# Optimization experiments

Measured on AMD Instinct MI355X. Metric: run time of the kernel, lower is better.

## Reference

```python
import jax, jax.numpy as jnp
import numpy as np

H, I, B = 256, 128, 512

def setup_inputs() -> dict:
    key = jax.random.key(0)
    ks = jax.random.split(key, 24)
    n = lambda k, shp, s=1.0: jax.random.normal(k, shp, dtype=jnp.float32) * s
    inp = {
        "x": n(ks[0], (B, I)),
        "hx": n(ks[1], (B, H), 0.1),
        "cx": n(ks[2], (B, H, H), 0.1),
        # input->gate weights (hidden, input), xavier-like scale
        "Wii": n(ks[3], (H, I), (2.0 / (H + I)) ** 0.5),
        "Wif": n(ks[4], (H, I), (2.0 / (H + I)) ** 0.5),
        "Wig": n(ks[5], (H, I), (2.0 / (H + I)) ** 0.5),
        "Wio": n(ks[6], (H, I), (2.0 / (H + I)) ** 0.5),
        # hidden->gate weights (hidden, hidden), ~orthogonal scale
        "Whi": n(ks[7], (H, H), H ** -0.5),
        "Whit": n(ks[8], (H, H), H ** -0.5),
        "Whf": n(ks[9], (H, H), H ** -0.5),
        "Whft": n(ks[10], (H, H), H ** -0.5),
        "Whc": n(ks[11], (H, H), H ** -0.5),
        "Whct": n(ks[12], (H, H), H ** -0.5),
        "Who": n(ks[13], (H, H), H ** -0.5),
        "Uinv": n(ks[14], (H, H), H ** -0.5),
        "Vtinv": n(ks[15], (H, H), H ** -0.5),
        # biases: bi/bf/bg are full (H,H) matrices, bo is (H,1)
        "bi": jnp.zeros((H, H), jnp.float32),
        "bf": jnp.zeros((H, H), jnp.float32),
        "bg": jnp.zeros((H, H), jnp.float32),
        "bo": jnp.zeros((H, 1), jnp.float32),
    }
    return inp


def reference(x, hx, cx, Wii, Wif, Wig, Wio, Whi, Whit, Whf, Whft, Whc, Whct, Who, Uinv, Vtinv, bi, bf, bg, bo):
    # W @ diag(v) @ M^T  ==  einsum('hi,bi,gi->bhg', W, v, M)
    def sandwich(Wx, Wh, Wht, b):
        # (Wx*x) @ Wx^T + (Wh*hx) @ Wht^T + b  -> (B,H,H)
        xt = jnp.einsum('hi,bi,gi->bhg', Wx, x, Wx)
        ht = jnp.einsum('hj,bj,gj->bhg', Wh, hx, Wht)
        return xt + ht + b

    i = jax.nn.sigmoid(sandwich(Wii, Whi, Whit, bi))
    f = jax.nn.sigmoid(sandwich(Wif, Whf, Whft, bf))
    g = jnp.tanh(sandwich(Wig, Whc, Whct, bg))
    # o: ordinary vector gate (B,H)
    o = jax.nn.sigmoid(jnp.einsum('hi,bi->bh', Wio, x)
                       + jnp.einsum('hj,bj->bh', Who, hx) + bo[:, 0])
    cx_new = f * cx + i * g                     # (B,H,H)
    # diag(Uinv @ cx_new @ Vtinv) per batch element -> (B,H)
    proj_down = jnp.einsum('ij,bjk,ki->bi', Uinv, cx_new, Vtinv)
    hx_new = o * jax.nn.sigmoid(proj_down)
    return hx_new
```

## Files before the change

### kernel.cpp

```cpp
#include <hip/hip_runtime.h>

#define Hh 256
#define Ii 128
#define Bb 512
#define KF 384
#define KB 64
#define LDB 40

typedef __attribute__((ext_vector_type(8))) short bf16x8;
typedef __attribute__((ext_vector_type(4))) float f32x4;
typedef unsigned short u16;
typedef unsigned int u32;

__device__ inline float bf2f(u16 u) { return __uint_as_float(((u32)u) << 16); }
__device__ inline u16 f2bf(float f) {
  u32 u = __float_as_uint(f);
  u += 0x7FFFu + ((u >> 16) & 1u);
  return (u16)(u >> 16);
}
__device__ inline float sigm(float x) { return 1.0f / (1.0f + __expf(-x)); }
__device__ inline float tanh_f(float x) { return 1.0f - 2.0f / (1.0f + __expf(2.0f * x)); }

__device__ inline int sp_idx(int j, int kk) {
  return j * 64 + ((((kk >> 3) ^ (j & 7)) << 3) | (kk & 7));
}

__global__ __launch_bounds__(256) void k_prep(
    const float* __restrict__ Wii, const float* __restrict__ Wif, const float* __restrict__ Wig,
    const float* __restrict__ Whi, const float* __restrict__ Whit,
    const float* __restrict__ Whf, const float* __restrict__ Whft,
    const float* __restrict__ Whc, const float* __restrict__ Whct,
    const float* __restrict__ Vtinv,
    u16* __restrict__ RW, u16* __restrict__ CW, u16* __restrict__ Vtt,
    float* __restrict__ proj) {
  const int tid = threadIdx.x, bx = blockIdx.x, y = blockIdx.y;
  if (y < 3) {
    const float* WX  = (y == 0) ? Wii : (y == 1 ? Wif : Wig);
    const float* WHr = (y == 0) ? Whi : (y == 1 ? Whf : Whc);
    const float* WHt = (y == 0) ? Whit : (y == 1 ? Whft : Whct);
    u16* rw = RW + y * Hh * KF;
    u16* cw = CW + y * Hh * KF;
#pragma unroll
    for (int it = 0; it < 4; ++it) {
      int idx = it * 24576 + bx * 256 + tid;
      int h = idx / KF, t = idx - h * KF;
      float a, c;
      if (t < Ii) { a = WX[h * Ii + t]; c = a; }
      else        { a = WHr[h * Hh + t - Ii]; c = WHt[h * Hh + t - Ii]; }
      rw[idx] = f2bf(a);
      cw[idx] = f2bf(c);
    }
  } else if (bx < 64) {
    __shared__ u16 tbuf[32][33];
    const int c = tid & 31, r8 = tid >> 5;
    const int tr = bx >> 3, tc = bx & 7;
#pragma unroll
    for (int rr = r8; rr < 32; rr += 8)
      tbuf[rr][c] = f2bf(Vtinv[(tc * 32 + rr) * Hh + tr * 32 + c]);
    __syncthreads();
#pragma unroll
    for (int rr = r8; rr < 32; rr += 8)
      Vtt[(tr * 32 + rr) * Hh + tc * 32 + c] = tbuf[c][rr];
  } else {
    const int base = (bx - 64) * 256 + tid;
    const float4 z = {0.f, 0.f, 0.f, 0.f};
#pragma unroll
    for (int it = 0; it < 4; ++it)
      *(float4*)(proj + (size_t)(it * 8192 + base) * 4) = z;
  }
}

template <int PHASE>
__device__ __forceinline__ void gate_pass(
    const u16* __restrict__ rw, const u16* __restrict__ cw,
    const float* __restrict__ bias, const float* __restrict__ cx_b,
    u16* sP, u16* sB, const float* sV, int tid, int k0) {
  const int lane = tid & 63, w = tid >> 6;
  const int r15 = lane & 15, quad = lane >> 4;
  const int brow = tid >> 2, bcg = tid & 3;

  f32x4 acc[4][4];
#pragma unroll
  for (int ti = 0; ti < 4; ++ti)
#pragma unroll
    for (int tk = 0; tk < 4; ++tk)
#pragma unroll
      for (int r = 0; r < 4; ++r) acc[ti][tk][r] = 0.0f;

  uint4 bnx = *(const uint4*)(cw + (k0 + brow) * KF + bcg * 8);
  bf16x8 fa[4];
#pragma unroll
  for (int ti = 0; ti < 4; ++ti)
    fa[ti] = *(const bf16x8*)(rw + (w * 64 + ti * 16 + r15) * KF + quad * 8);
  if (PHASE == 0) __syncthreads();
  {
    union { uint4 v; u16 u[8]; } in, ov;
    in.v = bnx;
    const float4 v0 = *(const float4*)(&sV[bcg * 8]);
    const float4 v1 = *(const float4*)(&sV[bcg * 8 + 4]);
    const float vs[8] = {v0.x, v0.y, v0.z, v0.w, v1.x, v1.y, v1.z, v1.w};
#pragma unroll
    for (int e = 0; e < 8; ++e) ov.u[e] = f2bf(bf2f(in.u[e]) * vs[e]);
    *(uint4*)(sB + brow * LDB + bcg * 8) = ov.v;
  }
  __syncthreads();

#pragma unroll
  for (int kc = 0; kc < 12; ++kc) {
    const int cur = kc & 1, nxt = cur ^ 1;
    uint4 bnx2;
    bf16x8 fan[4];
    if (kc < 11) {
      bnx2 = *(const uint4*)(cw + (k0 + brow) * KF + (kc + 1) * 32 + bcg * 8);
#pragma unroll
      for (int ti = 0; ti < 4; ++ti)
        fan[ti] = *(const bf16x8*)(rw + (w * 64 + ti * 16 + r15) * KF + (kc + 1) * 32 + quad * 8);
    }
    bf16x8 fb[4];
#pragma unroll
    for (int tk = 0; tk < 4; ++tk)
      fb[tk] = *(const bf16x8*)(&sB[cur * (KB * LDB) + (tk * 16 + r15) * LDB + quad * 8]);
#pragma unroll
    for (int ti = 0; ti < 4; ++ti)
#pragma unroll
      for (int tk = 0; tk < 4; ++tk)
        acc[ti][tk] = __builtin_amdgcn_mfma_f32_16x16x32_bf16(fa[ti], fb[tk], acc[ti][tk], 0, 0, 0);
    if (kc < 11) {
      union { uint4 v; u16 u[8]; } in, ov;
      in.v = bnx2;
      const float4 v0 = *(const float4*)(&sV[(kc + 1) * 32 + bcg * 8]);
      const float4 v1 = *(const float4*)(&sV[(kc + 1) * 32 + bcg * 8 + 4]);
      const float vs[8] = {v0.x, v0.y, v0.z, v0.w, v1.x, v1.y, v1.z, v1.w};
#pragma unroll
      for (int e = 0; e < 8; ++e) ov.u[e] = f2bf(bf2f(in.u[e]) * vs[e]);
      *(uint4*)(sB + nxt * (KB * LDB) + brow * LDB + bcg * 8) = ov.v;
#pragma unroll
      for (int ti = 0; ti < 4; ++ti) fa[ti] = fan[ti];
    }
    __syncthreads();
  }

#pragma unroll
  for (int ti = 0; ti < 4; ++ti) {
#pragma unroll
    for (int tk = 0; tk < 4; ++tk) {
#pragma unroll
      for (int r = 0; r < 4; ++r) {
        const int j = w * 64 + ti * 16 + quad * 4 + r;
        const int kk = tk * 16 + r15;
        const int si = sp_idx(j, kk);
        float z = acc[ti][tk][r] + bias[j * Hh + k0 + kk];
        if (PHASE == 0) {
          sP[si] = f2bf(tanh_f(z));
        } else if (PHASE == 1) {
          sP[si] = f2bf(sigm(z) * bf2f(sP[si]));
        } else {
          sP[si] = f2bf(sigm(z) * cx_b[j * Hh + k0 + kk] + bf2f(sP[si]));
        }
      }
    }
  }
}

__global__ __launch_bounds__(256, 3) void k_main(
    const float* __restrict__ x, const float* __restrict__ hx, const float* __restrict__ cx,
    const float* __restrict__ bi, const float* __restrict__ bfm, const float* __restrict__ bg,
    const float* __restrict__ Uinv, const u16* __restrict__ RW, const u16* __restrict__ CW,
    const u16* __restrict__ Vtt, float* __restrict__ proj) {
  __shared__ u16 sP[Hh * 64];
  __shared__ u16 sB[2 * KB * LDB];
  __shared__ float sV[KF];

  const int tid  = threadIdx.x;
  const int b    = blockIdx.x >> 2;
  const int k0   = (blockIdx.x & 3) * KB;
  const int lane = tid & 63;
  const int w    = tid >> 6;
  const int r15  = lane & 15;
  const int quad = lane >> 4;

  if (tid < Ii) sV[tid] = x[b * Ii + tid];
  sV[Ii + tid] = hx[b * Hh + tid];

  const float* cx_b = cx + (size_t)b * Hh * Hh;
  gate_pass<0>(RW + 2 * Hh * KF, CW + 2 * Hh * KF, bg,  cx_b, sP, sB, sV, tid, k0);
  gate_pass<1>(RW + 0 * Hh * KF, CW + 0 * Hh * KF, bi,  cx_b, sP, sB, sV, tid, k0);
  gate_pass<2>(RW + 1 * Hh * KF, CW + 1 * Hh * KF, bfm, cx_b, sP, sB, sV, tid, k0);

  __syncthreads();

  bf16x8 va[4][2];
#pragma unroll
  for (int ti = 0; ti < 4; ++ti)
#pragma unroll
    for (int ks = 0; ks < 2; ++ks)
      va[ti][ks] = *(const bf16x8*)(Vtt + (w * 64 + ti * 16 + r15) * Hh + k0 + ks * 32 + quad * 8);

  float racc[4][4];
#pragma unroll
  for (int ti = 0; ti < 4; ++ti)
#pragma unroll
    for (int r = 0; r < 4; ++r) racc[ti][r] = 0.0f;

  for (int jt = 0; jt < 4; ++jt) {
    f32x4 pacc[4][4];
#pragma unroll
    for (int ti = 0; ti < 4; ++ti)
#pragma unroll
      for (int tj = 0; tj < 4; ++tj)
#pragma unroll
        for (int r = 0; r < 4; ++r) pacc[ti][tj][r] = 0.0f;
#pragma unroll
    for (int ks = 0; ks < 2; ++ks) {
      bf16x8 fbp[4];
#pragma unroll
      for (int tj = 0; tj < 4; ++tj) {
        const int j = jt * 64 + tj * 16 + r15;
        const int ch = (ks * 4 + quad) ^ (j & 7);
        fbp[tj] = *(const bf16x8*)(&sP[j * 64 + ch * 8]);
      }
#pragma unroll
      for (int ti = 0; ti < 4; ++ti)
#pragma unroll
        for (int tj = 0; tj < 4; ++tj)
          pacc[ti][tj] = __builtin_amdgcn_mfma_f32_16x16x32_bf16(va[ti][ks], fbp[tj], pacc[ti][tj], 0, 0, 0);
    }
#pragma unroll
    for (int ti = 0; ti < 4; ++ti)
#pragma unroll
      for (int tj = 0; tj < 4; ++tj)
#pragma unroll
        for (int r = 0; r < 4; ++r) {
          const int i  = w * 64 + ti * 16 + quad * 4 + r;
          const int jj = jt * 64 + tj * 16 + r15;
          racc[ti][r] += pacc[ti][tj][r] * Uinv[i * Hh + jj];
        }
  }

#pragma unroll
  for (int ti = 0; ti < 4; ++ti)
#pragma unroll
    for (int r = 0; r < 4; ++r) {
      float v = racc[ti][r];
      v += __shfl_xor(v, 1);
      v += __shfl_xor(v, 2);
      v += __shfl_xor(v, 4);
      v += __shfl_xor(v, 8);
      if (r15 == 0) atomicAdd(&proj[b * Hh + w * 64 + ti * 16 + quad * 4 + r], v);
    }
}

__global__ __launch_bounds__(256) void k_out(
    const float* __restrict__ x, const float* __restrict__ hx,
    const float* __restrict__ Wio, const float* __restrict__ Who,
    const float* __restrict__ bo, const float* __restrict__ proj,
    float* __restrict__ out) {
  __shared__ float sv[KF];
  const int b = blockIdx.x, tid = threadIdx.x;
  const int lane = tid & 63, w = tid >> 6;
  if (tid < Ii) sv[tid] = x[b * Ii + tid];
  sv[Ii + tid] = hx[b * Hh + tid];
  __syncthreads();
  for (int rr = 0; rr < 64; ++rr) {
    const int h = w * 64 + rr;
    float p = Wio[h * Ii + lane]        * sv[lane]
            + Wio[h * Ii + 64 + lane]   * sv[64 + lane]
            + Who[h * Hh + lane]        * sv[128 + lane]
            + Who[h * Hh + 64 + lane]   * sv[192 + lane]
            + Who[h * Hh + 128 + lane]  * sv[256 + lane]
            + Who[h * Hh + 192 + lane]  * sv[320 + lane];
    p += __shfl_xor(p, 32);
    p += __shfl_xor(p, 16);
    p += __shfl_xor(p, 8);
    p += __shfl_xor(p, 4);
    p += __shfl_xor(p, 2);
    p += __shfl_xor(p, 1);
    if (lane == 0)
      out[b * Hh + h] = sigm(p + bo[h]) * sigm(proj[b * Hh + h]);
  }
}

extern "C" void kernel_launch(void* const* d_in, const int* in_sizes, int n_in,
                              void* d_out, int out_size, void* d_ws, size_t ws_size,
                              hipStream_t stream) {
  (void)in_sizes; (void)n_in; (void)out_size; (void)ws_size;
  const float* x    = (const float*)d_in[0];
  const float* hx   = (const float*)d_in[1];
  const float* cx   = (const float*)d_in[2];
  const float* Wii  = (const float*)d_in[3];
  const float* Wif  = (const float*)d_in[4];
  const float* Wig  = (const float*)d_in[5];
  const float* Wio  = (const float*)d_in[6];
  const float* Whi  = (const float*)d_in[7];
  const float* Whit = (const float*)d_in[8];
  const float* Whf  = (const float*)d_in[9];
  const float* Whft = (const float*)d_in[10];
  const float* Whc  = (const float*)d_in[11];
  const float* Whct = (const float*)d_in[12];
  const float* Who  = (const float*)d_in[13];
  const float* Uinv = (const float*)d_in[14];
  const float* Vtinv= (const float*)d_in[15];
  const float* bi   = (const float*)d_in[16];
  const float* bf   = (const float*)d_in[17];
  const float* bg   = (const float*)d_in[18];
  const float* bo   = (const float*)d_in[19];
  float* out = (float*)d_out;

  u16* RW  = (u16*)d_ws;
  u16* CW  = RW + 3 * Hh * KF;
  u16* Vtt = CW + 3 * Hh * KF;
  float* proj = (float*)(Vtt + Hh * Hh);

  k_prep<<<dim3(96, 4), 256, 0, stream>>>(Wii, Wif, Wig, Whi, Whit, Whf, Whft, Whc, Whct,
                                          Vtinv, RW, CW, Vtt, proj);
  k_main<<<2048, 256, 0, stream>>>(x, hx, cx, bi, bf, bg, Uinv, RW, CW, Vtt, proj);
  k_out<<<512, 256, 0, stream>>>(x, hx, Wio, Who, bo, proj, out);
}
```

Before: 582.7 us.

## Split gate rows across blocks, keep gate state in registers, prepack bias

Each k_main block now covers 128 gate rows instead of 256, so the grid doubles and shared memory per block halves, allowing four blocks per CU. Intermediate gate values (tanh g, i*g) now stay in registers across phases rather than being written to and reread from shared memory. Biases are converted once to bf16 in the prep kernel and stored in a per-thread fragment order, so each thread reads them as vector loads. Costs are twice the atomics on proj, duplicated B-operand staging in each block, and bf16 rounding of the bias.

New measurement: 868.6 us. +49.1%, slower.

```diff
diff --git a/kernel.cpp b/kernel.cpp
--- a/kernel.cpp
+++ b/kernel.cpp
@@ -1,4 +1,5 @@
 #include <hip/hip_runtime.h>
+#include <hip/hip_bf16.h>
 
 #define Hh 256
 #define Ii 128
@@ -18,6 +19,10 @@
   u += 0x7FFFu + ((u >> 16) & 1u);
   return (u16)(u >> 16);
 }
+__device__ inline u32 pack_bf16x2(float a, float b) {
+  __hip_bfloat162 h = __float22bfloat162_rn(make_float2(a, b));
+  u32 r; __builtin_memcpy(&r, &h, 4); return r;
+}
 __device__ inline float sigm(float x) { return 1.0f / (1.0f + __expf(-x)); }
 __device__ inline float tanh_f(float x) { return 1.0f - 2.0f / (1.0f + __expf(2.0f * x)); }
 
@@ -31,8 +36,9 @@
     const float* __restrict__ Whf, const float* __restrict__ Whft,
     const float* __restrict__ Whc, const float* __restrict__ Whct,
     const float* __restrict__ Vtinv,
+    const float* __restrict__ bi, const float* __restrict__ bfm, const float* __restrict__ bg,
     u16* __restrict__ RW, u16* __restrict__ CW, u16* __restrict__ Vtt,
-    float* __restrict__ proj) {
+    u16* __restrict__ biasP, float* __restrict__ proj) {
   const int tid = threadIdx.x, bx = blockIdx.x, y = blockIdx.y;
   if (y < 3) {
     const float* WX  = (y == 0) ? Wii : (y == 1 ? Wif : Wig);
@@ -50,144 +56,185 @@
       rw[idx] = f2bf(a);
       cw[idx] = f2bf(c);
     }
-  } else if (bx < 64) {
-    __shared__ u16 tbuf[32][33];
-    const int c = tid & 31, r8 = tid >> 5;
-    const int tr = bx >> 3, tc = bx & 7;
-#pragma unroll
-    for (int rr = r8; rr < 32; rr += 8)
-      tbuf[rr][c] = f2bf(Vtinv[(tc * 32 + rr) * Hh + tr * 32 + c]);
-    __syncthreads();
-#pragma unroll
-    for (int rr = r8; rr < 32; rr += 8)
-      Vtt[(tr * 32 + rr) * Hh + tc * 32 + c] = tbuf[c][rr];
+  } else if (y == 3) {
+    if (bx < 64) {
+      __shared__ u16 tbuf[32][33];
+      const int c = tid & 31, r8 = tid >> 5;
+      const int tr = bx >> 3, tc = bx & 7;
+#pragma unroll
+      for (int rr = r8; rr < 32; rr += 8)
+        tbuf[rr][c] = f2bf(Vtinv[(tc * 32 + rr) * Hh + tr * 32 + c]);
+      __syncthreads();
+#pragma unroll
+      for (int rr = r8; rr < 32; rr += 8)
+        Vtt[(tr * 32 + rr) * Hh + tc * 32 + c] = tbuf[c][rr];
+    } else if (bx < 96) {
+      const int base = (bx - 64) * 256 + tid;
+      const float4 z = {0.f, 0.f, 0.f, 0.f};
+#pragma unroll
+      for (int it = 0; it < 4; ++it)
+        *(float4*)(proj + (size_t)(it * 8192 + base) * 4) = z;
+    }
   } else {
-    const int base = (bx - 64) * 256 + tid;
-    const float4 z = {0.f, 0.f, 0.f, 0.f};
-#pragma unroll
-    for (int it = 0; it < 4; ++it)
-      *(float4*)(proj + (size_t)(it * 8192 + base) * 4) = z;
+    const int base = (bx * 256 + tid) * 8;
+#pragma unroll
+    for (int e8 = 0; e8 < 8; ++e8) {
+      int f = base + e8;
+      int g = f >> 16;
+      int r1 = f & 65535;
+      int jb = r1 >> 15;
+      int r2 = r1 & 32767;
+      int kb = r2 >> 13;
+      int r3 = r2 & 8191;
+      int t  = r3 >> 5;
+      int e  = r3 & 31;
+      int w = t >> 6, quad = (t >> 4) & 3, r15 = t & 15;
+      int ti = e >> 4, tk = (e >> 2) & 3, rr = e & 3;
+      int j   = jb * 128 + w * 32 + ti * 16 + quad * 4 + rr;
+      int col = kb * 64 + tk * 16 + r15;
+      const float* src = (g == 0) ? bg : (g == 1 ? bi : bfm);
+      biasP[f] = f2bf(src[j * Hh + col]);
+    }
   }
 }
 
-template <int PHASE>
-__device__ __forceinline__ void gate_pass(
-    const u16* __restrict__ rw, const u16* __restrict__ cw,
-    const float* __restrict__ bias, const float* __restrict__ cx_b,
-    u16* sP, u16* sB, const float* sV, int tid, int k0) {
-  const int lane = tid & 63, w = tid >> 6;
-  const int r15 = lane & 15, quad = lane >> 4;
-  const int brow = tid >> 2, bcg = tid & 3;
-
-  f32x4 acc[4][4];
-#pragma unroll
-  for (int ti = 0; ti < 4; ++ti)
-#pragma unroll
-    for (int tk = 0; tk < 4; ++tk)
-#pragma unroll
-      for (int r = 0; r < 4; ++r) acc[ti][tk][r] = 0.0f;
-
-  uint4 bnx = *(const uint4*)(cw + (k0 + brow) * KF + bcg * 8);
-  bf16x8 fa[4];
-#pragma unroll
-  for (int ti = 0; ti < 4; ++ti)
-    fa[ti] = *(const bf16x8*)(rw + (w * 64 + ti * 16 + r15) * KF + quad * 8);
-  if (PHASE == 0) __syncthreads();
-  {
-    union { uint4 v; u16 u[8]; } in, ov;
-    in.v = bnx;
-    const float4 v0 = *(const float4*)(&sV[bcg * 8]);
-    const float4 v1 = *(const float4*)(&sV[bcg * 8 + 4]);
-    const float vs[8] = {v0.x, v0.y, v0.z, v0.w, v1.x, v1.y, v1.z, v1.w};
-#pragma unroll
-    for (int e = 0; e < 8; ++e) ov.u[e] = f2bf(bf2f(in.u[e]) * vs[e]);
-    *(uint4*)(sB + brow * LDB + bcg * 8) = ov.v;
-  }
-  __syncthreads();
-
-#pragma unroll
-  for (int kc = 0; kc < 12; ++kc) {
-    const int cur = kc & 1, nxt = cur ^ 1;
-    uint4 bnx2;
-    bf16x8 fan[4];
-    if (kc < 11) {
-      bnx2 = *(const uint4*)(cw + (k0 + brow) * KF + (kc + 1) * 32 + bcg * 8);
-#pragma unroll
-      for (int ti = 0; ti < 4; ++ti)
-        fan[ti] = *(const bf16x8*)(rw + (w * 64 + ti * 16 + r15) * KF + (kc + 1) * 32 + quad * 8);
-    }
-    bf16x8 fb[4];
-#pragma unroll
-    for (int tk = 0; tk < 4; ++tk)
-      fb[tk] = *(const bf16x8*)(&sB[cur * (KB * LDB) + (tk * 16 + r15) * LDB + quad * 8]);
-#pragma unroll
-    for (int ti = 0; ti < 4; ++ti)
-#pragma unroll
-      for (int tk = 0; tk < 4; ++tk)
-        acc[ti][tk] = __builtin_amdgcn_mfma_f32_16x16x32_bf16(fa[ti], fb[tk], acc[ti][tk], 0, 0, 0);
-    if (kc < 11) {
-      union { uint4 v; u16 u[8]; } in, ov;
-      in.v = bnx2;
-      const float4 v0 = *(const float4*)(&sV[(kc + 1) * 32 + bcg * 8]);
-      const float4 v1 = *(const float4*)(&sV[(kc + 1) * 32 + bcg * 8 + 4]);
-      const float vs[8] = {v0.x, v0.y, v0.z, v0.w, v1.x, v1.y, v1.z, v1.w};
-#pragma unroll
-      for (int e = 0; e < 8; ++e) ov.u[e] = f2bf(bf2f(in.u[e]) * vs[e]);
-      *(uint4*)(sB + nxt * (KB * LDB) + brow * LDB + bcg * 8) = ov.v;
-#pragma unroll
-      for (int ti = 0; ti < 4; ++ti) fa[ti] = fan[ti];
-    }
-    __syncthreads();
-  }
-
-#pragma unroll
-  for (int ti = 0; ti < 4; ++ti) {
-#pragma unroll
-    for (int tk = 0; tk < 4; ++tk) {
-#pragma unroll
-      for (int r = 0; r < 4; ++r) {
-        const int j = w * 64 + ti * 16 + quad * 4 + r;
-        const int kk = tk * 16 + r15;
-        const int si = sp_idx(j, kk);
-        float z = acc[ti][tk][r] + bias[j * Hh + k0 + kk];
-        if (PHASE == 0) {
-          sP[si] = f2bf(tanh_f(z));
-        } else if (PHASE == 1) {
-          sP[si] = f2bf(sigm(z) * bf2f(sP[si]));
-        } else {
-          sP[si] = f2bf(sigm(z) * cx_b[j * Hh + k0 + kk] + bf2f(sP[si]));
-        }
-      }
-    }
-  }
-}
-
-__global__ __launch_bounds__(256, 3) void k_main(
+__global__ __launch_bounds__(256, 4) void k_main(
     const float* __restrict__ x, const float* __restrict__ hx, const float* __restrict__ cx,
-    const float* __restrict__ bi, const float* __restrict__ bfm, const float* __restrict__ bg,
     const float* __restrict__ Uinv, const u16* __restrict__ RW, const u16* __restrict__ CW,
-    const u16* __restrict__ Vtt, float* __restrict__ proj) {
-  __shared__ u16 sP[Hh * 64];
+    const u16* __restrict__ Vtt, const u16* __restrict__ biasP, float* __restrict__ proj) {
+  __shared__ u16 sP[128 * 64];
   __shared__ u16 sB[2 * KB * LDB];
   __shared__ float sV[KF];
 
   const int tid  = threadIdx.x;
-  const int b    = blockIdx.x >> 2;
-  const int k0   = (blockIdx.x & 3) * KB;
+  const int b    = blockIdx.x >> 3;
+  const int jb   = (blockIdx.x >> 2) & 1;
+  const int kb   = blockIdx.x & 3;
+  const int k0   = kb * KB;
   const int lane = tid & 63;
   const int w    = tid >> 6;
   const int r15  = lane & 15;
   const int quad = lane >> 4;
+  const int jbase = jb * 128 + w * 32;
+  const int brow = tid >> 2, bcg = tid & 3;
 
   if (tid < Ii) sV[tid] = x[b * Ii + tid];
   sV[Ii + tid] = hx[b * Hh + tid];
-
-  const float* cx_b = cx + (size_t)b * Hh * Hh;
-  gate_pass<0>(RW + 2 * Hh * KF, CW + 2 * Hh * KF, bg,  cx_b, sP, sB, sV, tid, k0);
-  gate_pass<1>(RW + 0 * Hh * KF, CW + 0 * Hh * KF, bi,  cx_b, sP, sB, sV, tid, k0);
-  gate_pass<2>(RW + 1 * Hh * KF, CW + 1 * Hh * KF, bfm, cx_b, sP, sB, sV, tid, k0);
-
   __syncthreads();
+
+  float p[2][4][4];
+  f32x4 acc[2][4];
+
+  for (int phase = 0; phase < 3; ++phase) {
+    const int g = (phase == 0) ? 2 : (phase == 1 ? 0 : 1);
+    const u16* rw = RW + g * Hh * KF;
+    const u16* cw = CW + g * Hh * KF;
+
+#pragma unroll
+    for (int ti = 0; ti < 2; ++ti)
+#pragma unroll
+      for (int tk = 0; tk < 4; ++tk)
+#pragma unroll
+        for (int r = 0; r < 4; ++r) acc[ti][tk][r] = 0.0f;
+
+    bf16x8 fa[2];
+#pragma unroll
+    for (int ti = 0; ti < 2; ++ti)
+      fa[ti] = *(const bf16x8*)(rw + (jbase + ti * 16 + r15) * KF + quad * 8);
+    {
+      union { uint4 v; u16 u[8]; } in;
+      union { uint4 v; u32 d[4]; } ov;
+      in.v = *(const uint4*)(cw + (k0 + brow) * KF + bcg * 8);
+      const float4 v0 = *(const float4*)(&sV[bcg * 8]);
+      const float4 v1 = *(const float4*)(&sV[bcg * 8 + 4]);
+      ov.d[0] = pack_bf16x2(bf2f(in.u[0]) * v0.x, bf2f(in.u[1]) * v0.y);
+      ov.d[1] = pack_bf16x2(bf2f(in.u[2]) * v0.z, bf2f(in.u[3]) * v0.w);
+      ov.d[2] = pack_bf16x2(bf2f(in.u[4]) * v1.x, bf2f(in.u[5]) * v1.y);
+      ov.d[3] = pack_bf16x2(bf2f(in.u[6]) * v1.z, bf2f(in.u[7]) * v1.w);
+      *(uint4*)(sB + brow * LDB + bcg * 8) = ov.v;
+    }
+    __syncthreads();
+
+#pragma unroll
+    for (int kc = 0; kc < 12; ++kc) {
+      const int cur = kc & 1, nxt = cur ^ 1;
+      uint4 bnx;
+      bf16x8 fan[2];
+      if (kc < 11) {
+        bnx = *(const uint4*)(cw + (k0 + brow) * KF + (kc + 1) * 32 + bcg * 8);
+#pragma unroll
+        for (int ti = 0; ti < 2; ++ti)
+          fan[ti] = *(const bf16x8*)(rw + (jbase + ti * 16 + r15) * KF + (kc + 1) * 32 + quad * 8);
+      }
+      bf16x8 fb[4];
+#pragma unroll
+      for (int tk = 0; tk < 4; ++tk)
+        fb[tk] = *(const bf16x8*)(&sB[cur * (KB * LDB) + (tk * 16 + r15) * LDB + quad * 8]);
+#pragma unroll
+      for (int ti = 0; ti < 2; ++ti)
+#pragma unroll
+        for (int tk = 0; tk < 4; ++tk)
+          acc[ti][tk] = __builtin_amdgcn_mfma_f32_16x16x32_bf16(fa[ti], fb[tk], acc[ti][tk], 0, 0, 0);
+      if (kc < 11) {
+        union { uint4 v; u16 u[8]; } in;
+        union { uint4 v; u32 d[4]; } ov;
+        in.v = bnx;
+        const float4 v0 = *(const float4*)(&sV[(kc + 1) * 32 + bcg * 8]);
+        const float4 v1 = *(const float4*)(&sV[(kc + 1) * 32 + bcg * 8 + 4]);
+        ov.d[0] = pack_bf16x2(bf2f(in.u[0]) * v0.x, bf2f(in.u[1]) * v0.y);
+        ov.d[1] = pack_bf16x2(bf2f(in.u[2]) * v0.z, bf2f(in.u[3]) * v0.w);
+        ov.d[2] = pack_bf16x2(bf2f(in.u[4]) * v1.x, bf2f(in.u[5]) * v1.y);
+        ov.d[3] = pack_bf16x2(bf2f(in.u[6]) * v1.z, bf2f(in.u[7]) * v1.w);
+        *(uint4*)(sB + nxt * (KB * LDB) + brow * LDB + bcg * 8) = ov.v;
+#pragma unroll
+        for (int ti = 0; ti < 2; ++ti) fa[ti] = fan[ti];
+      }
+      __syncthreads();
+    }
+
+    union { uint4 v[4]; u16 u[32]; } bb;
+    {
+      const u16* bp = biasP + (((size_t)(phase * 2 + jb) * 4 + kb) * 256 + tid) * 32;
+#pragma unroll
+      for (int q = 0; q < 4; ++q) bb.v[q] = *(const uint4*)(bp + q * 8);
+    }
+    if (phase == 2) {
+      const float* cx_b = cx + (size_t)b * Hh * Hh;
+      float cxv[2][4][4];
+#pragma unroll
+      for (int ti = 0; ti < 2; ++ti)
+#pragma unroll
+        for (int tk = 0; tk < 4; ++tk)
+#pragma unroll
+          for (int r = 0; r < 4; ++r)
+            cxv[ti][tk][r] = cx_b[(jbase + ti * 16 + quad * 4 + r) * Hh + k0 + tk * 16 + r15];
+#pragma unroll
+      for (int ti = 0; ti < 2; ++ti)
+#pragma unroll
+        for (int tk = 0; tk < 4; ++tk)
+#pragma unroll
+          for (int r = 0; r < 4; ++r) {
+            const int e = ti * 16 + tk * 4 + r;
+            float z = acc[ti][tk][r] + bf2f(bb.u[e]);
+            float c = sigm(z) * cxv[ti][tk][r] + p[ti][tk][r];
+            const int jl = w * 32 + ti * 16 + quad * 4 + r;
+            const int kk = tk * 16 + r15;
+            sP[sp_idx(jl, kk)] = f2bf(c);
+          }
+    } else {
+#pragma unroll
+      for (int ti = 0; ti < 2; ++ti)
+#pragma unroll
+        for (int tk = 0; tk < 4; ++tk)
+#pragma unroll
+          for (int r = 0; r < 4; ++r) {
+            const int e = ti * 16 + tk * 4 + r;
+            float z = acc[ti][tk][r] + bf2f(bb.u[e]);
+            if (phase == 0) p[ti][tk][r] = tanh_f(z);
+            else            p[ti][tk][r] *= sigm(z);
+          }
+    }
+  }
 
   bf16x8 va[4][2];
 #pragma unroll
@@ -195,6 +242,7 @@
 #pragma unroll
     for (int ks = 0; ks < 2; ++ks)
       va[ti][ks] = *(const bf16x8*)(Vtt + (w * 64 + ti * 16 + r15) * Hh + k0 + ks * 32 + quad * 8);
+  __syncthreads();
 
   float racc[4][4];
 #pragma unroll
@@ -202,39 +250,37 @@
 #pragma unroll
     for (int r = 0; r < 4; ++r) racc[ti][r] = 0.0f;
 
-  for (int jt = 0; jt < 4; ++jt) {
-    f32x4 pacc[4][4];
-#pragma unroll
-    for (int ti = 0; ti < 4; ++ti)
-#pragma unroll
-      for (int tj = 0; tj < 4; ++tj)
-#pragma unroll
-        for (int r = 0; r < 4; ++r) pacc[ti][tj][r] = 0.0f;
-#pragma unroll
-    for (int ks = 0; ks < 2; ++ks) {
-      bf16x8 fbp[4];
+  for (int jt = 0; jt < 2; ++jt) {
+    bf16x8 fbp[2][4];
+#pragma unroll
+    for (int ks = 0; ks < 2; ++ks)
 #pragma unroll
       for (int tj = 0; tj < 4; ++tj) {
         const int j = jt * 64 + tj * 16 + r15;
         const int ch = (ks * 4 + quad) ^ (j & 7);
-        fbp[tj] = *(const bf16x8*)(&sP[j * 64 + ch * 8]);
+        fbp[ks][tj] = *(const bf16x8*)(&sP[j * 64 + ch * 8]);
       }
 #pragma unroll
-      for (int ti = 0; ti < 4; ++ti)
+    for (int ti = 0; ti < 4; ++ti) {
+      f32x4 pacc[4];
+#pragma unroll
+      for (int tj = 0; tj < 4; ++tj)
+#pragma unroll
+        for (int r = 0; r < 4; ++r) pacc[tj][r] = 0.0f;
+#pragma unroll
+      for (int ks = 0; ks < 2; ++ks)
 #pragma unroll
         for (int tj = 0; tj < 4; ++tj)
-          pacc[ti][tj] = __builtin_amdgcn_mfma_f32_16x16x32_bf16(va[ti][ks], fbp[tj], pacc[ti][tj], 0, 0, 0);
-    }
-#pragma unroll
-    for (int ti = 0; ti < 4; ++ti)
+          pacc[tj] = __builtin_amdgcn_mfma_f32_16x16x32_bf16(va[ti][ks], fbp[ks][tj], pacc[tj], 0, 0, 0);
 #pragma unroll
       for (int tj = 0; tj < 4; ++tj)
 #pragma unroll
         for (int r = 0; r < 4; ++r) {
           const int i  = w * 64 + ti * 16 + quad * 4 + r;
-          const int jj = jt * 64 + tj * 16 + r15;
-          racc[ti][r] += pacc[ti][tj][r] * Uinv[i * Hh + jj];
+          const int jj = jb * 128 + jt * 64 + tj * 16 + r15;
+          racc[ti][r] += pacc[tj][r] * Uinv[i * Hh + jj];
         }
+    }
   }
 
 #pragma unroll
@@ -306,13 +352,14 @@
   const float* bo   = (const float*)d_in[19];
   float* out = (float*)d_out;
 
-  u16* RW  = (u16*)d_ws;
-  u16* CW  = RW + 3 * Hh * KF;
-  u16* Vtt = CW + 3 * Hh * KF;
-  float* proj = (float*)(Vtt + Hh * Hh);
-
-  k_prep<<<dim3(96, 4), 256, 0, stream>>>(Wii, Wif, Wig, Whi, Whit, Whf, Whft, Whc, Whct,
-                                          Vtinv, RW, CW, Vtt, proj);
-  k_main<<<2048, 256, 0, stream>>>(x, hx, cx, bi, bf, bg, Uinv, RW, CW, Vtt, proj);
+  u16* RW    = (u16*)d_ws;
+  u16* CW    = RW + 3 * Hh * KF;
+  u16* Vtt   = CW + 3 * Hh * KF;
+  u16* biasP = Vtt + Hh * Hh;
+  float* proj = (float*)(biasP + 3 * Hh * Hh);
+
+  k_prep<<<dim3(96, 5), 256, 0, stream>>>(Wii, Wif, Wig, Whi, Whit, Whf, Whft, Whc, Whct,
+                                          Vtinv, bi, bf, bg, RW, CW, Vtt, biasP, proj);
+  k_main<<<4096, 256, 0, stream>>>(x, hx, cx, Uinv, RW, CW, Vtt, biasP, proj);
   k_out<<<512, 256, 0, stream>>>(x, hx, Wio, Who, bo, proj, out);
 }
```
